# Kernel tuning notes

Hardware: AMD Instinct MI355X
Metric: run time of the kernel (lower is better)

Reference implementation:

```python
import jax, jax.numpy as jnp
import numpy as np

D_MODEL = 1024
NUM_HEADS = 16
D_K = D_MODEL // NUM_HEADS
LN_EPS = 1e-5


def setup_inputs() -> dict:
    key = jax.random.key(0)
    ks = jax.random.split(key, 10)
    s = 1.0 / np.sqrt(D_MODEL)
    x = jax.random.normal(ks[0], (4, 2048, D_MODEL), dtype=jnp.float32)
    Wq = jax.random.uniform(ks[1], (D_MODEL, D_MODEL), jnp.float32, -s, s)
    bq = jax.random.uniform(ks[2], (D_MODEL,), jnp.float32, -s, s)
    Wk = jax.random.uniform(ks[3], (D_MODEL, D_MODEL), jnp.float32, -s, s)
    bk = jax.random.uniform(ks[4], (D_MODEL,), jnp.float32, -s, s)
    Wv = jax.random.uniform(ks[5], (D_MODEL, D_MODEL), jnp.float32, -s, s)
    bv = jax.random.uniform(ks[6], (D_MODEL,), jnp.float32, -s, s)
    Wo = jax.random.uniform(ks[7], (D_MODEL, D_MODEL), jnp.float32, -s, s)
    bo = jax.random.uniform(ks[8], (D_MODEL,), jnp.float32, -s, s)
    gamma = jnp.ones((D_MODEL,), jnp.float32)
    beta = jnp.zeros((D_MODEL,), jnp.float32)
    return {"x": x, "Wq": Wq, "bq": bq, "Wk": Wk, "bk": bk, "Wv": Wv,
            "bv": bv, "Wo": Wo, "bo": bo, "gamma": gamma, "beta": beta}


def reference(x, Wq, bq, Wk, bk, Wv, bv, Wo, bo, gamma, beta):
    B, S, D = x.shape
    H, dk = NUM_HEADS, D_K
    # torch Linear: y = x @ W.T + b
    def proj(W, b):
        y = jnp.einsum('bsd,ed->bse', x, W) + b
        return y.reshape(B, S, H, dk).transpose(0, 2, 1, 3)  # [B,H,S,dk]
    Q = proj(Wq, bq)
    K = proj(Wk, bk)
    V = proj(Wv, bv)
    scores = jnp.einsum('bhqd,bhkd->bhqk', Q, K) / np.sqrt(dk)
    attn = jax.nn.softmax(scores, axis=-1)
    head = jnp.einsum('bhqk,bhkd->bhqd', attn, V)
    head = head.transpose(0, 2, 1, 3).reshape(B, S, D)
    out = jnp.einsum('bsd,ed->bse', head, Wo) + bo
    # LayerNorm
    mu = jnp.mean(out, axis=-1, keepdims=True)
    var = jnp.var(out, axis=-1, keepdims=True)
    out = (out - mu) * jax.lax.rsqrt(var + LN_EPS) * gamma + beta
    # dropout is identity in eval mode
    return x + out
```

## Files before the change

kernel.cpp:

```cpp
#include <hip/hip_runtime.h>
#include <stdint.h>

typedef unsigned short u16;
typedef unsigned int u32;
typedef __attribute__((ext_vector_type(8))) short short8;
typedef __attribute__((ext_vector_type(4))) short short4b;
typedef __attribute__((ext_vector_type(4))) float f32x4;
typedef __attribute__((ext_vector_type(4))) unsigned short u16x4;

#define DEV static __device__ __forceinline__

DEV float bf2f(u16 b) { return __uint_as_float(((uint32_t)b) << 16); }
DEV u16 f2bf(float f) {
  uint32_t u = __float_as_uint(f);
  u += 0x7FFFu + ((u >> 16) & 1u);
  return (u16)(u >> 16);
}
DEV void gld16(const u16* gsrc, u16* ldsdst) {
  __builtin_amdgcn_global_load_lds((const __attribute__((address_space(1))) void*)gsrc,
                                   (__attribute__((address_space(3))) void*)ldsdst, 16, 0, 0);
}
#define MFMA16(a, b, c) __builtin_amdgcn_mfma_f32_16x16x32_bf16(a, b, c, 0, 0, 0)

#define WAITVM4() asm volatile("s_waitcnt vmcnt(4)" ::: "memory")
#define WAITVM0() asm volatile("s_waitcnt vmcnt(0)" ::: "memory")
DEV void barrier() {
  asm volatile("" ::: "memory");
  __builtin_amdgcn_s_barrier();
  asm volatile("" ::: "memory");
}

#if __has_builtin(__builtin_amdgcn_mfma_f32_16x16x16bf16_1k)
DEV f32x4 mfma_k16(short4b a, short4b b, f32x4 c) {
  return __builtin_amdgcn_mfma_f32_16x16x16bf16_1k(a, b, c, 0, 0, 0);
}
#else
DEV f32x4 mfma_k16(short4b a, short4b b, f32x4 c) {
  f32x4 d;
  asm volatile("v_mfma_f32_16x16x16_bf16 %0, %1, %2, %3"
               : "=&v"(d) : "v"(a), "v"(b), "v"(c));
  return d;
}
#endif

#if __has_builtin(__builtin_amdgcn_exp2f)
DEV float fexp2(float x) { return __builtin_amdgcn_exp2f(x); }
#else
DEV float fexp2(float x) { return exp2f(x); }
#endif

DEV u32 cvtpk(float lo, float hi) {
  u32 r;
  asm("v_cvt_pk_bf16_f32 %0, %1, %2" : "=v"(r) : "v"(lo), "v"(hi));
  return r;
}

DEV f32x4 v4max(f32x4 a, f32x4 b) {
  f32x4 r;
  r.x = fmaxf(a.x, b.x); r.y = fmaxf(a.y, b.y);
  r.z = fmaxf(a.z, b.z); r.w = fmaxf(a.w, b.w);
  return r;
}

__global__ __launch_bounds__(256) void k_convert(
    const float* __restrict__ x, const float* __restrict__ wq, const float* __restrict__ wk,
    const float* __restrict__ wv, const float* __restrict__ wo, u16* __restrict__ ws)
{
  int bid = blockIdx.x, t = threadIdx.x;
  const float* src; u16* dst; size_t off;
  if (bid < 8192) { src = x; dst = ws; off = (size_t)bid * 1024; }
  else {
    int r = bid - 8192; int sel = r >> 10; int lb = r & 1023;
    src = sel == 0 ? wq : sel == 1 ? wk : sel == 2 ? wv : wo;
    dst = ws + 8388608u + (size_t)sel * 1048576u;
    off = (size_t)lb * 1024;
  }
  size_t e = off + (size_t)t * 4;
  f32x4 v = *(const f32x4*)(src + e);
  u16x4 o;
  o.x = f2bf(v.x); o.y = f2bf(v.y); o.z = f2bf(v.z); o.w = f2bf(v.w);
  *(u16x4*)(dst + e) = o;
}

DEV void gemm_mainloop(const u16* __restrict__ A, const u16* __restrict__ B,
                       int m0, int n0, u16* As, u16* Bs, f32x4 acc[4][4])
{
  const int tid = threadIdx.x, lane = tid & 63, w = tid >> 6;
  const int fr = lane & 15, g = lane >> 4;
  const int wm = w >> 1, wn = w & 1;

  const int rowA0 = (w * 2 + 0) * 16 + (lane >> 2);
  const int rowA1 = (w * 2 + 1) * 16 + (lane >> 2);
  const int ci = lane & 3;
  const u16* ga0 = A + (size_t)(m0 + rowA0) * 1024 + ((ci ^ (rowA0 & 3)) << 3);
  const u16* ga1 = A + (size_t)(m0 + rowA1) * 1024 + ((ci ^ (rowA1 & 3)) << 3);
  const u16* gb0 = B + (size_t)(n0 + rowA0) * 1024 + ((ci ^ (rowA0 & 3)) << 3);
  const u16* gb1 = B + (size_t)(n0 + rowA1) * 1024 + ((ci ^ (rowA1 & 3)) << 3);
  u16* lA0 = As + (w * 2 + 0) * 512;
  u16* lA1 = As + (w * 2 + 1) * 512;
  u16* lB0 = Bs + (w * 2 + 0) * 512;
  u16* lB1 = Bs + (w * 2 + 1) * 512;

  int raf[4], rbf[4];
#pragma unroll
  for (int i = 0; i < 4; ++i) {
    int rA = wm * 64 + i * 16 + fr;
    raf[i] = rA * 32 + ((g ^ (rA & 3)) << 3);
    int rB = wn * 64 + i * 16 + fr;
    rbf[i] = rB * 32 + ((g ^ (rB & 3)) << 3);
  }

  for (int k0 = 0; k0 < 1024; k0 += 32) {
    __syncthreads();
    gld16(ga0 + k0, lA0);
    gld16(ga1 + k0, lA1);
    gld16(gb0 + k0, lB0);
    gld16(gb1 + k0, lB1);
    __syncthreads();
    short8 af[4], bf[4];
#pragma unroll
    for (int i = 0; i < 4; ++i) af[i] = *(const short8*)&As[raf[i]];
#pragma unroll
    for (int i = 0; i < 4; ++i) bf[i] = *(const short8*)&Bs[rbf[i]];
#pragma unroll
    for (int mi = 0; mi < 4; ++mi)
#pragma unroll
      for (int ni = 0; ni < 4; ++ni)
        acc[mi][ni] = MFMA16(af[mi], bf[ni], acc[mi][ni]);
  }
}

__global__ __launch_bounds__(256) void k_gemm_qkv(
    const u16* __restrict__ xb, const u16* __restrict__ wqb, const u16* __restrict__ wkb,
    const u16* __restrict__ wvb, const float* __restrict__ bq, const float* __restrict__ bk,
    const float* __restrict__ bv, u16* __restrict__ Qg, u16* __restrict__ Kg,
    u16* __restrict__ Vtg)
{
  __shared__ u16 As[128 * 32], Bs[128 * 32];
  const int mb = blockIdx.x, nb_all = blockIdx.y;
  const int mat = nb_all >> 3, nb = nb_all & 7;
  const u16* W = mat == 0 ? wqb : (mat == 1 ? wkb : wvb);
  const float* bias = mat == 0 ? bq : (mat == 1 ? bk : bv);
  const int m0 = mb * 128, n0 = nb * 128;

  f32x4 acc[4][4];
  f32x4 z = {0.f, 0.f, 0.f, 0.f};
#pragma unroll
  for (int i = 0; i < 4; ++i)
#pragma unroll
    for (int j = 0; j < 4; ++j) acc[i][j] = z;

  gemm_mainloop(xb, W, m0, n0, As, Bs, acc);

  const int tid = threadIdx.x, lane = tid & 63, w = tid >> 6;
  const int fr = lane & 15, g = lane >> 4;
  const int wm = w >> 1, wn = w & 1;

  if (mat <= 1) {
    u16* Og = mat == 0 ? Qg : Kg;
    const float scale = mat == 0 ? 0.18033688011112042f : 1.0f;
#pragma unroll
    for (int mi = 0; mi < 4; ++mi)
#pragma unroll
      for (int ni = 0; ni < 4; ++ni) {
        int n = n0 + wn * 64 + ni * 16 + fr;
        float bv_ = bias[n];
        int h = n >> 6, d = n & 63;
#pragma unroll
        for (int r = 0; r < 4; ++r) {
          int m = m0 + wm * 64 + mi * 16 + 4 * g + r;
          int b = m >> 11, s = m & 2047;
          float v = (acc[mi][ni][r] + bv_) * scale;
          Og[(((size_t)(b * 16 + h)) * 2048 + (size_t)s) * 64 + d] = f2bf(v);
        }
      }
  } else {
#pragma unroll
    for (int mi = 0; mi < 4; ++mi)
#pragma unroll
      for (int ni = 0; ni < 4; ++ni) {
        int n = n0 + wn * 64 + ni * 16 + fr;
        float bv_ = bias[n];
        int h = n >> 6, d = n & 63;
        int mbase = m0 + wm * 64 + mi * 16 + 4 * g;
        int b = mbase >> 11, s0 = mbase & 2047;
        u16x4 pk;
        pk.x = f2bf(acc[mi][ni][0] + bv_);
        pk.y = f2bf(acc[mi][ni][1] + bv_);
        pk.z = f2bf(acc[mi][ni][2] + bv_);
        pk.w = f2bf(acc[mi][ni][3] + bv_);
        *(u16x4*)&Vtg[(((size_t)(b * 16 + h)) * 64 + d) * 2048 + s0] = pk;
      }
  }
}

__global__ __launch_bounds__(512, 1) void k_attn(
    const u16* __restrict__ Qg, const u16* __restrict__ Kg, const u16* __restrict__ Vtg,
    u16* __restrict__ headb)
{
  __shared__ u16 K_lds[2][128 * 64];
  __shared__ u16 V_lds[2][64 * 128];
  const int tid = threadIdx.x, lane = tid & 63, w = tid >> 6;
  const int fr = lane & 15, g = lane >> 4;
  const int swz = ((blockIdx.x & 7) << 6) + (blockIdx.x >> 3);
  const int qb = swz & 7, bh = swz >> 3;
  const u16* Qbase = Qg + (size_t)bh * 2048 * 64;
  const u16* Kbase = Kg + (size_t)bh * 2048 * 64;
  const u16* Vbase = Vtg + (size_t)bh * 64 * 2048;

  const int ck0 = w * 2, ck1 = w * 2 + 1;
  const int krow0 = ck0 * 8 + (lane >> 3), krow1 = ck1 * 8 + (lane >> 3);
  const int kci = lane & 7;
  const u16* gk0 = Kbase + (size_t)krow0 * 64 + ((kci ^ (krow0 & 7)) << 3);
  const u16* gk1 = Kbase + (size_t)krow1 * 64 + ((kci ^ (krow1 & 7)) << 3);
  const int vrow0 = ck0 * 4 + (lane >> 4), vrow1 = ck1 * 4 + (lane >> 4);
  const int vci = lane & 15;
  const u16* gv0 = Vbase + (size_t)vrow0 * 2048 + ((vci ^ (vrow0 & 7)) << 3);
  const u16* gv1 = Vbase + (size_t)vrow1 * 2048 + ((vci ^ (vrow1 & 7)) << 3);

  short8 qf[2][2];
#pragma unroll
  for (int mi = 0; mi < 2; ++mi)
#pragma unroll
    for (int kt = 0; kt < 2; ++kt) {
      int qrow = qb * 256 + w * 32 + mi * 16 + fr;
      qf[mi][kt] = *(const short8*)&Qbase[(size_t)qrow * 64 + kt * 32 + g * 8];
    }

  f32x4 po[2][4];
  f32x4 z = {0.f, 0.f, 0.f, 0.f};
#pragma unroll
  for (int mi = 0; mi < 2; ++mi)
#pragma unroll
    for (int dt = 0; dt < 4; ++dt) po[mi][dt] = z;
  float mrun[2] = {-1e30f, -1e30f};
  float lrun[2] = {0.f, 0.f};

  gld16(gk0, K_lds[0] + ck0 * 512);
  gld16(gk1, K_lds[0] + ck1 * 512);
  gld16(gv0, V_lds[0] + ck0 * 512);
  gld16(gv1, V_lds[0] + ck1 * 512);

  for (int kv = 0; kv < 16; ++kv) {
    const int cur = kv & 1;
    if (kv < 15) {
      const int ko = (kv + 1) * 128 * 64;
      const int vo = (kv + 1) * 128;
      gld16(gk0 + ko, K_lds[cur ^ 1] + ck0 * 512);
      gld16(gk1 + ko, K_lds[cur ^ 1] + ck1 * 512);
      gld16(gv0 + vo, V_lds[cur ^ 1] + ck0 * 512);
      gld16(gv1 + vo, V_lds[cur ^ 1] + ck1 * 512);
      WAITVM4();
    } else {
      WAITVM0();
    }
    barrier();
    const u16* Kc = K_lds[cur];
    const u16* Vc = V_lds[cur];

    f32x4 sc[2][8];
#pragma unroll
    for (int mi = 0; mi < 2; ++mi)
#pragma unroll
      for (int nt = 0; nt < 8; ++nt) sc[mi][nt] = z;
    __builtin_amdgcn_s_setprio(1);
#pragma unroll
    for (int nt = 0; nt < 8; ++nt) {
      int rk = nt * 16 + fr;
#pragma unroll
      for (int kt = 0; kt < 2; ++kt) {
        short8 kb = *(const short8*)&Kc[rk * 64 + (((kt * 4 + g) ^ (rk & 7)) << 3)];
        sc[0][nt] = MFMA16(kb, qf[0][kt], sc[0][nt]);
        sc[1][nt] = MFMA16(kb, qf[1][kt], sc[1][nt]);
      }
    }
    __builtin_amdgcn_s_setprio(0);

    short4b pa[2][8];
#pragma unroll
    for (int mi = 0; mi < 2; ++mi) {
      f32x4 m4 = sc[mi][0];
#pragma unroll
      for (int nt = 1; nt < 8; ++nt) m4 = v4max(m4, sc[mi][nt]);
      float mx = fmaxf(fmaxf(m4.x, m4.y), fmaxf(m4.z, m4.w));
      mx = fmaxf(mx, __shfl_xor(mx, 16, 64));
      mx = fmaxf(mx, __shfl_xor(mx, 32, 64));
      const bool defer = __all(mx - mrun[mi] <= 8.0f);
      const float mnew = defer ? mrun[mi] : mx;
      f32x4 s4 = z;
#pragma unroll
      for (int nt = 0; nt < 8; ++nt) {
        f32x4 p;
        p.x = fexp2(sc[mi][nt].x - mnew);
        p.y = fexp2(sc[mi][nt].y - mnew);
        p.z = fexp2(sc[mi][nt].z - mnew);
        p.w = fexp2(sc[mi][nt].w - mnew);
        sc[mi][nt] = p;
        s4 += p;
      }
      float rs = (s4.x + s4.y) + (s4.z + s4.w);
      rs += __shfl_xor(rs, 16, 64);
      rs += __shfl_xor(rs, 32, 64);
      if (defer) {
        lrun[mi] += rs;
      } else {
        float alpha = fexp2(mrun[mi] - mnew);
        lrun[mi] = lrun[mi] * alpha + rs;
        mrun[mi] = mnew;
        f32x4 al4;
#pragma unroll
        for (int r = 0; r < 4; ++r) al4[r] = __shfl(alpha, 4 * g + r, 64);
#pragma unroll
        for (int dt = 0; dt < 4; ++dt) po[mi][dt] *= al4;
      }
#pragma unroll
      for (int nt = 0; nt < 8; ++nt) {
        union { u32 u[2]; short4b s; } cv;
        cv.u[0] = cvtpk(sc[mi][nt].x, sc[mi][nt].y);
        cv.u[1] = cvtpk(sc[mi][nt].z, sc[mi][nt].w);
        pa[mi][nt] = cv.s;
      }
    }

    __builtin_amdgcn_s_setprio(1);
#pragma unroll
    for (int nt = 0; nt < 8; ++nt) {
#pragma unroll
      for (int dt = 0; dt < 4; ++dt) {
        int d = dt * 16 + fr;
        short4b vb = *(const short4b*)&Vc[d * 128 + ((((nt << 1) | (g >> 1)) ^ (d & 7)) << 3) + ((g & 1) << 2)];
        po[0][dt] = mfma_k16(pa[0][nt], vb, po[0][dt]);
        po[1][dt] = mfma_k16(pa[1][nt], vb, po[1][dt]);
      }
    }
    __builtin_amdgcn_s_setprio(0);
    barrier();
  }

  float linv[2][4];
#pragma unroll
  for (int mi = 0; mi < 2; ++mi)
#pragma unroll
    for (int r = 0; r < 4; ++r)
      linv[mi][r] = 1.0f / __shfl(lrun[mi], 4 * g + r, 64);

  const int b = bh >> 4, h = bh & 15;
#pragma unroll
  for (int mi = 0; mi < 2; ++mi)
#pragma unroll
    for (int dt = 0; dt < 4; ++dt)
#pragma unroll
      for (int r = 0; r < 4; ++r) {
        int srow = qb * 256 + w * 32 + mi * 16 + 4 * g + r;
        float v = po[mi][dt][r] * linv[mi][r];
        int e = h * 64 + dt * 16 + fr;
        headb[((size_t)(b * 2048 + srow)) * 1024 + e] = f2bf(v);
      }
}

__global__ __launch_bounds__(256) void k_gemm_o(
    const u16* __restrict__ headb, const u16* __restrict__ wob, const float* __restrict__ bo,
    u16* __restrict__ projb)
{
  __shared__ u16 As[128 * 32], Bs[128 * 32];
  const int m0 = blockIdx.x * 128, n0 = blockIdx.y * 128;
  f32x4 acc[4][4];
  f32x4 z = {0.f, 0.f, 0.f, 0.f};
#pragma unroll
  for (int i = 0; i < 4; ++i)
#pragma unroll
    for (int j = 0; j < 4; ++j) acc[i][j] = z;

  gemm_mainloop(headb, wob, m0, n0, As, Bs, acc);

  const int tid = threadIdx.x, lane = tid & 63, w = tid >> 6;
  const int fr = lane & 15, g = lane >> 4;
  const int wm = w >> 1, wn = w & 1;
#pragma unroll
  for (int mi = 0; mi < 4; ++mi)
#pragma unroll
    for (int ni = 0; ni < 4; ++ni) {
      int n = n0 + wn * 64 + ni * 16 + fr;
      float bv_ = bo[n];
#pragma unroll
      for (int r = 0; r < 4; ++r) {
        int m = m0 + wm * 64 + mi * 16 + 4 * g + r;
        projb[(size_t)m * 1024 + n] = f2bf(acc[mi][ni][r] + bv_);
      }
    }
}

__global__ __launch_bounds__(256) void k_ln(
    const u16* __restrict__ projb, const float* __restrict__ x,
    const float* __restrict__ gamma, const float* __restrict__ beta, float* __restrict__ out)
{
  __shared__ float sh1[4], sh2[4];
  const int row = blockIdx.x, t = threadIdx.x, lane = t & 63, w = t >> 6;
  const size_t base = (size_t)row * 1024;
  u16x4 pv = *(const u16x4*)&projb[base + t * 4];
  float v0 = bf2f(pv.x), v1 = bf2f(pv.y), v2 = bf2f(pv.z), v3 = bf2f(pv.w);
  float s1 = v0 + v1 + v2 + v3;
  float s2 = v0 * v0 + v1 * v1 + v2 * v2 + v3 * v3;
  for (int m = 1; m < 64; m <<= 1) {
    s1 += __shfl_xor(s1, m, 64);
    s2 += __shfl_xor(s2, m, 64);
  }
  if (lane == 0) { sh1[w] = s1; sh2[w] = s2; }
  __syncthreads();
  s1 = sh1[0] + sh1[1] + sh1[2] + sh1[3];
  s2 = sh2[0] + sh2[1] + sh2[2] + sh2[3];
  float mu = s1 * (1.0f / 1024.0f);
  float var = s2 * (1.0f / 1024.0f) - mu * mu;
  float rsd = rsqrtf(var + 1e-5f);
  f32x4 xv = *(const f32x4*)&x[base + t * 4];
  f32x4 res;
  int e = t * 4;
  res.x = xv.x + (v0 - mu) * rsd * gamma[e + 0] + beta[e + 0];
  res.y = xv.y + (v1 - mu) * rsd * gamma[e + 1] + beta[e + 1];
  res.z = xv.z + (v2 - mu) * rsd * gamma[e + 2] + beta[e + 2];
  res.w = xv.w + (v3 - mu) * rsd * gamma[e + 3] + beta[e + 3];
  *(f32x4*)&out[base + t * 4] = res;
}

extern "C" void kernel_launch(void* const* d_in, const int* in_sizes, int n_in,
                              void* d_out, int out_size, void* d_ws, size_t ws_size,
                              hipStream_t stream)
{
  const float* x     = (const float*)d_in[0];
  const float* Wq    = (const float*)d_in[1];
  const float* bq    = (const float*)d_in[2];
  const float* Wk    = (const float*)d_in[3];
  const float* bk    = (const float*)d_in[4];
  const float* Wv    = (const float*)d_in[5];
  const float* bv    = (const float*)d_in[6];
  const float* Wo    = (const float*)d_in[7];
  const float* bo    = (const float*)d_in[8];
  const float* gamma = (const float*)d_in[9];
  const float* beta  = (const float*)d_in[10];
  float* out = (float*)d_out;

  u16* ws   = (u16*)d_ws;
  u16* xb   = ws;
  u16* wqb  = ws + 8388608;
  u16* wkb  = wqb + 1048576;
  u16* wvb  = wkb + 1048576;
  u16* wob  = wvb + 1048576;
  u16* Qg   = wob + 1048576;
  u16* Kg   = Qg + 8388608;
  u16* Vtg  = Kg + 8388608;
  u16* headb = Vtg + 8388608;
  u16* projb = Qg;

  k_convert<<<12288, 256, 0, stream>>>(x, Wq, Wk, Wv, Wo, ws);
  k_gemm_qkv<<<dim3(64, 24), 256, 0, stream>>>(xb, wqb, wkb, wvb, bq, bk, bv, Qg, Kg, Vtg);
  k_attn<<<dim3(512), 512, 0, stream>>>(Qg, Kg, Vtg, headb);
  k_gemm_o<<<dim3(64, 8), 256, 0, stream>>>(headb, wob, bo, projb);
  k_ln<<<8192, 256, 0, stream>>>(projb, x, gamma, beta, out);
}
```

Measured before the change: 241.7 us.

## Rewrite attention kernel with 32x32x16 MFMA and smaller 64-key tiles

Moves the flash-attention kernel from 16x16 MFMA tiles to 32x32x16 bf16 MFMA. Each wave now owns 32 query rows, so row max and sum reductions need only one cross-half shuffle, and the P fragments are rebuilt through a lane-xor exchange. Blocks shrink to 256 threads with 128 queries each, the KV tile drops to 64 keys, and the grid doubles to 1024 blocks. The aim is fewer MFMA issues and less softmax shuffle overhead, plus higher occupancy. The cost is twice as many KV-loop iterations and barriers, and extra shuffles to repack P.

```diff
diff --git a/kernel.cpp b/kernel.cpp
--- a/kernel.cpp
+++ b/kernel.cpp
@@ -4,8 +4,8 @@
 typedef unsigned short u16;
 typedef unsigned int u32;
 typedef __attribute__((ext_vector_type(8))) short short8;
-typedef __attribute__((ext_vector_type(4))) short short4b;
 typedef __attribute__((ext_vector_type(4))) float f32x4;
+typedef __attribute__((ext_vector_type(16))) float f32x16;
 typedef __attribute__((ext_vector_type(4))) unsigned short u16x4;
 
 #define DEV static __device__ __forceinline__
@@ -21,6 +21,7 @@
                                    (__attribute__((address_space(3))) void*)ldsdst, 16, 0, 0);
 }
 #define MFMA16(a, b, c) __builtin_amdgcn_mfma_f32_16x16x32_bf16(a, b, c, 0, 0, 0)
+#define MFMA32(a, b, c) __builtin_amdgcn_mfma_f32_32x32x16_bf16(a, b, c, 0, 0, 0)
 
 #define WAITVM4() asm volatile("s_waitcnt vmcnt(4)" ::: "memory")
 #define WAITVM0() asm volatile("s_waitcnt vmcnt(0)" ::: "memory")
@@ -30,19 +31,6 @@
   asm volatile("" ::: "memory");
 }
 
-#if __has_builtin(__builtin_amdgcn_mfma_f32_16x16x16bf16_1k)
-DEV f32x4 mfma_k16(short4b a, short4b b, f32x4 c) {
-  return __builtin_amdgcn_mfma_f32_16x16x16bf16_1k(a, b, c, 0, 0, 0);
-}
-#else
-DEV f32x4 mfma_k16(short4b a, short4b b, f32x4 c) {
-  f32x4 d;
-  asm volatile("v_mfma_f32_16x16x16_bf16 %0, %1, %2, %3"
-               : "=&v"(d) : "v"(a), "v"(b), "v"(c));
-  return d;
-}
-#endif
-
 #if __has_builtin(__builtin_amdgcn_exp2f)
 DEV float fexp2(float x) { return __builtin_amdgcn_exp2f(x); }
 #else
@@ -52,13 +40,6 @@
 DEV u32 cvtpk(float lo, float hi) {
   u32 r;
   asm("v_cvt_pk_bf16_f32 %0, %1, %2" : "=v"(r) : "v"(lo), "v"(hi));
-  return r;
-}
-
-DEV f32x4 v4max(f32x4 a, f32x4 b) {
-  f32x4 r;
-  r.x = fmaxf(a.x, b.x); r.y = fmaxf(a.y, b.y);
-  r.z = fmaxf(a.z, b.z); r.w = fmaxf(a.w, b.w);
   return r;
 }
 
@@ -194,58 +175,57 @@
   }
 }
 
-__global__ __launch_bounds__(512, 1) void k_attn(
+__global__ __launch_bounds__(256) void k_attn(
     const u16* __restrict__ Qg, const u16* __restrict__ Kg, const u16* __restrict__ Vtg,
     u16* __restrict__ headb)
 {
-  __shared__ u16 K_lds[2][128 * 64];
-  __shared__ u16 V_lds[2][64 * 128];
+  __shared__ u16 K_lds[2][64 * 64];
+  __shared__ u16 V_lds[2][64 * 64];
   const int tid = threadIdx.x, lane = tid & 63, w = tid >> 6;
-  const int fr = lane & 15, g = lane >> 4;
-  const int swz = ((blockIdx.x & 7) << 6) + (blockIdx.x >> 3);
-  const int qb = swz & 7, bh = swz >> 3;
+  const int l31 = lane & 31, h5 = lane >> 5, k7 = lane & 7;
+  const bool lo_half = (h5 == 0);
+  const int swz = ((blockIdx.x & 7) << 7) + (blockIdx.x >> 3);
+  const int qb = swz & 15, bh = swz >> 4;
   const u16* Qbase = Qg + (size_t)bh * 2048 * 64;
   const u16* Kbase = Kg + (size_t)bh * 2048 * 64;
   const u16* Vbase = Vtg + (size_t)bh * 64 * 2048;
 
   const int ck0 = w * 2, ck1 = w * 2 + 1;
-  const int krow0 = ck0 * 8 + (lane >> 3), krow1 = ck1 * 8 + (lane >> 3);
-  const int kci = lane & 7;
-  const u16* gk0 = Kbase + (size_t)krow0 * 64 + ((kci ^ (krow0 & 7)) << 3);
-  const u16* gk1 = Kbase + (size_t)krow1 * 64 + ((kci ^ (krow1 & 7)) << 3);
-  const int vrow0 = ck0 * 4 + (lane >> 4), vrow1 = ck1 * 4 + (lane >> 4);
-  const int vci = lane & 15;
-  const u16* gv0 = Vbase + (size_t)vrow0 * 2048 + ((vci ^ (vrow0 & 7)) << 3);
-  const u16* gv1 = Vbase + (size_t)vrow1 * 2048 + ((vci ^ (vrow1 & 7)) << 3);
-
-  short8 qf[2][2];
-#pragma unroll
-  for (int mi = 0; mi < 2; ++mi)
-#pragma unroll
-    for (int kt = 0; kt < 2; ++kt) {
-      int qrow = qb * 256 + w * 32 + mi * 16 + fr;
-      qf[mi][kt] = *(const short8*)&Qbase[(size_t)qrow * 64 + kt * 32 + g * 8];
-    }
-
-  f32x4 po[2][4];
-  f32x4 z = {0.f, 0.f, 0.f, 0.f};
-#pragma unroll
-  for (int mi = 0; mi < 2; ++mi)
-#pragma unroll
-    for (int dt = 0; dt < 4; ++dt) po[mi][dt] = z;
-  float mrun[2] = {-1e30f, -1e30f};
-  float lrun[2] = {0.f, 0.f};
+  const int srow0 = ck0 * 8 + (lane >> 3), srow1 = ck1 * 8 + (lane >> 3);
+  const int sci = lane & 7;
+  const u16* gk0 = Kbase + (size_t)srow0 * 64 + ((sci ^ (srow0 & 7)) << 3);
+  const u16* gk1 = Kbase + (size_t)srow1 * 64 + ((sci ^ (srow1 & 7)) << 3);
+  const u16* gv0 = Vbase + (size_t)srow0 * 2048 + ((sci ^ (srow0 & 7)) << 3);
+  const u16* gv1 = Vbase + (size_t)srow1 * 2048 + ((sci ^ (srow1 & 7)) << 3);
+
+  short8 qf[4];
+  {
+    const u16* qrow = Qbase + (size_t)(qb * 128 + w * 32 + l31) * 64;
+#pragma unroll
+    for (int j = 0; j < 4; ++j)
+      qf[j] = *(const short8*)&qrow[j * 16 + h5 * 8];
+  }
+
+  int cj[4];
+#pragma unroll
+  for (int j = 0; j < 4; ++j) cj[j] = (((2 * j + h5) ^ k7) << 3);
+  const int rb = l31 * 64;
+
+  f32x16 po0, po1;
+#pragma unroll
+  for (int e = 0; e < 16; ++e) { po0[e] = 0.f; po1[e] = 0.f; }
+  float mrun = -1e30f, lrun = 0.f;
 
   gld16(gk0, K_lds[0] + ck0 * 512);
   gld16(gk1, K_lds[0] + ck1 * 512);
   gld16(gv0, V_lds[0] + ck0 * 512);
   gld16(gv1, V_lds[0] + ck1 * 512);
 
-  for (int kv = 0; kv < 16; ++kv) {
+  for (int kv = 0; kv < 32; ++kv) {
     const int cur = kv & 1;
-    if (kv < 15) {
-      const int ko = (kv + 1) * 128 * 64;
-      const int vo = (kv + 1) * 128;
+    if (kv < 31) {
+      const int ko = (kv + 1) * 64 * 64;
+      const int vo = (kv + 1) * 64;
       gld16(gk0 + ko, K_lds[cur ^ 1] + ck0 * 512);
       gld16(gk1 + ko, K_lds[cur ^ 1] + ck1 * 512);
       gld16(gv0 + vo, V_lds[cur ^ 1] + ck0 * 512);
@@ -258,104 +238,99 @@
     const u16* Kc = K_lds[cur];
     const u16* Vc = V_lds[cur];
 
-    f32x4 sc[2][8];
-#pragma unroll
-    for (int mi = 0; mi < 2; ++mi)
-#pragma unroll
-      for (int nt = 0; nt < 8; ++nt) sc[mi][nt] = z;
+    f32x16 s0, s1;
+#pragma unroll
+    for (int e = 0; e < 16; ++e) { s0[e] = 0.f; s1[e] = 0.f; }
     __builtin_amdgcn_s_setprio(1);
 #pragma unroll
-    for (int nt = 0; nt < 8; ++nt) {
-      int rk = nt * 16 + fr;
-#pragma unroll
-      for (int kt = 0; kt < 2; ++kt) {
-        short8 kb = *(const short8*)&Kc[rk * 64 + (((kt * 4 + g) ^ (rk & 7)) << 3)];
-        sc[0][nt] = MFMA16(kb, qf[0][kt], sc[0][nt]);
-        sc[1][nt] = MFMA16(kb, qf[1][kt], sc[1][nt]);
-      }
+    for (int j = 0; j < 4; ++j) {
+      short8 kf0 = *(const short8*)&Kc[rb + cj[j]];
+      short8 kf1 = *(const short8*)&Kc[2048 + rb + cj[j]];
+      s0 = MFMA32(kf0, qf[j], s0);
+      s1 = MFMA32(kf1, qf[j], s1);
     }
     __builtin_amdgcn_s_setprio(0);
 
-    short4b pa[2][8];
-#pragma unroll
-    for (int mi = 0; mi < 2; ++mi) {
-      f32x4 m4 = sc[mi][0];
-#pragma unroll
-      for (int nt = 1; nt < 8; ++nt) m4 = v4max(m4, sc[mi][nt]);
-      float mx = fmaxf(fmaxf(m4.x, m4.y), fmaxf(m4.z, m4.w));
-      mx = fmaxf(mx, __shfl_xor(mx, 16, 64));
-      mx = fmaxf(mx, __shfl_xor(mx, 32, 64));
-      const bool defer = __all(mx - mrun[mi] <= 8.0f);
-      const float mnew = defer ? mrun[mi] : mx;
-      f32x4 s4 = z;
-#pragma unroll
-      for (int nt = 0; nt < 8; ++nt) {
-        f32x4 p;
-        p.x = fexp2(sc[mi][nt].x - mnew);
-        p.y = fexp2(sc[mi][nt].y - mnew);
-        p.z = fexp2(sc[mi][nt].z - mnew);
-        p.w = fexp2(sc[mi][nt].w - mnew);
-        sc[mi][nt] = p;
-        s4 += p;
-      }
-      float rs = (s4.x + s4.y) + (s4.z + s4.w);
-      rs += __shfl_xor(rs, 16, 64);
-      rs += __shfl_xor(rs, 32, 64);
-      if (defer) {
-        lrun[mi] += rs;
-      } else {
-        float alpha = fexp2(mrun[mi] - mnew);
-        lrun[mi] = lrun[mi] * alpha + rs;
-        mrun[mi] = mnew;
-        f32x4 al4;
-#pragma unroll
-        for (int r = 0; r < 4; ++r) al4[r] = __shfl(alpha, 4 * g + r, 64);
-#pragma unroll
-        for (int dt = 0; dt < 4; ++dt) po[mi][dt] *= al4;
-      }
-#pragma unroll
-      for (int nt = 0; nt < 8; ++nt) {
-        union { u32 u[2]; short4b s; } cv;
-        cv.u[0] = cvtpk(sc[mi][nt].x, sc[mi][nt].y);
-        cv.u[1] = cvtpk(sc[mi][nt].z, sc[mi][nt].w);
-        pa[mi][nt] = cv.s;
-      }
+    float mx = fmaxf(s0[0], s1[0]);
+#pragma unroll
+    for (int e = 1; e < 16; ++e) mx = fmaxf(mx, fmaxf(s0[e], s1[e]));
+    mx = fmaxf(mx, __shfl_xor(mx, 32, 64));
+    const bool defer = __all(mx - mrun <= 8.0f);
+    const float mnew = defer ? mrun : mx;
+#pragma unroll
+    for (int e = 0; e < 16; ++e) {
+      s0[e] = fexp2(s0[e] - mnew);
+      s1[e] = fexp2(s1[e] - mnew);
+    }
+    float a0 = 0.f, a1 = 0.f, a2 = 0.f, a3 = 0.f;
+#pragma unroll
+    for (int e = 0; e < 4; ++e) {
+      a0 += s0[4 * e + 0] + s1[4 * e + 0];
+      a1 += s0[4 * e + 1] + s1[4 * e + 1];
+      a2 += s0[4 * e + 2] + s1[4 * e + 2];
+      a3 += s0[4 * e + 3] + s1[4 * e + 3];
+    }
+    float rs = (a0 + a1) + (a2 + a3);
+    rs += __shfl_xor(rs, 32, 64);
+    if (defer) {
+      lrun += rs;
+    } else {
+      float alpha = fexp2(mrun - mnew);
+      lrun = lrun * alpha + rs;
+      mrun = mnew;
+#pragma unroll
+      for (int e = 0; e < 16; ++e) { po0[e] *= alpha; po1[e] *= alpha; }
     }
 
     __builtin_amdgcn_s_setprio(1);
 #pragma unroll
-    for (int nt = 0; nt < 8; ++nt) {
-#pragma unroll
-      for (int dt = 0; dt < 4; ++dt) {
-        int d = dt * 16 + fr;
-        short4b vb = *(const short4b*)&Vc[d * 128 + ((((nt << 1) | (g >> 1)) ^ (d & 7)) << 3) + ((g & 1) << 2)];
-        po[0][dt] = mfma_k16(pa[0][nt], vb, po[0][dt]);
-        po[1][dt] = mfma_k16(pa[1][nt], vb, po[1][dt]);
-      }
+    for (int s = 0; s < 4; ++s) {
+      u32 lo0, lo1, hi0, hi1;
+      if (s == 0)      { lo0 = cvtpk(s0[0], s0[1]);  lo1 = cvtpk(s0[2], s0[3]);
+                         hi0 = cvtpk(s0[4], s0[5]);  hi1 = cvtpk(s0[6], s0[7]); }
+      else if (s == 1) { lo0 = cvtpk(s0[8], s0[9]);  lo1 = cvtpk(s0[10], s0[11]);
+                         hi0 = cvtpk(s0[12], s0[13]); hi1 = cvtpk(s0[14], s0[15]); }
+      else if (s == 2) { lo0 = cvtpk(s1[0], s1[1]);  lo1 = cvtpk(s1[2], s1[3]);
+                         hi0 = cvtpk(s1[4], s1[5]);  hi1 = cvtpk(s1[6], s1[7]); }
+      else             { lo0 = cvtpk(s1[8], s1[9]);  lo1 = cvtpk(s1[10], s1[11]);
+                         hi0 = cvtpk(s1[12], s1[13]); hi1 = cvtpk(s1[14], s1[15]); }
+      u32 sent0 = lo_half ? hi0 : lo0;
+      u32 sent1 = lo_half ? hi1 : lo1;
+      u32 r0 = __shfl_xor(sent0, 32, 64);
+      u32 r1 = __shfl_xor(sent1, 32, 64);
+      union { u32 u[4]; short8 v; } pf;
+      pf.u[0] = lo_half ? lo0 : r0;
+      pf.u[1] = lo_half ? lo1 : r1;
+      pf.u[2] = lo_half ? r0 : hi0;
+      pf.u[3] = lo_half ? r1 : hi1;
+      short8 vf0 = *(const short8*)&Vc[rb + cj[s]];
+      short8 vf1 = *(const short8*)&Vc[2048 + rb + cj[s]];
+      po0 = MFMA32(vf0, pf.v, po0);
+      po1 = MFMA32(vf1, pf.v, po1);
     }
     __builtin_amdgcn_s_setprio(0);
     barrier();
   }
 
-  float linv[2][4];
-#pragma unroll
-  for (int mi = 0; mi < 2; ++mi)
-#pragma unroll
-    for (int r = 0; r < 4; ++r)
-      linv[mi][r] = 1.0f / __shfl(lrun[mi], 4 * g + r, 64);
-
+  const float linv = 1.0f / lrun;
   const int b = bh >> 4, h = bh & 15;
-#pragma unroll
-  for (int mi = 0; mi < 2; ++mi)
-#pragma unroll
-    for (int dt = 0; dt < 4; ++dt)
-#pragma unroll
-      for (int r = 0; r < 4; ++r) {
-        int srow = qb * 256 + w * 32 + mi * 16 + 4 * g + r;
-        float v = po[mi][dt][r] * linv[mi][r];
-        int e = h * 64 + dt * 16 + fr;
-        headb[((size_t)(b * 2048 + srow)) * 1024 + e] = f2bf(v);
-      }
+  const int srow = qb * 128 + w * 32 + l31;
+  u16* rowp = headb + (size_t)(b * 2048 + srow) * 1024 + h * 64;
+#pragma unroll
+  for (int i = 0; i < 4; ++i) {
+    u16x4 pk;
+    pk.x = f2bf(po0[4 * i + 0] * linv);
+    pk.y = f2bf(po0[4 * i + 1] * linv);
+    pk.z = f2bf(po0[4 * i + 2] * linv);
+    pk.w = f2bf(po0[4 * i + 3] * linv);
+    *(u16x4*)&rowp[8 * i + 4 * h5] = pk;
+    u16x4 pk2;
+    pk2.x = f2bf(po1[4 * i + 0] * linv);
+    pk2.y = f2bf(po1[4 * i + 1] * linv);
+    pk2.z = f2bf(po1[4 * i + 2] * linv);
+    pk2.w = f2bf(po1[4 * i + 3] * linv);
+    *(u16x4*)&rowp[32 + 8 * i + 4 * h5] = pk2;
+  }
 }
 
 __global__ __launch_bounds__(256) void k_gemm_o(
@@ -453,7 +428,7 @@
 
   k_convert<<<12288, 256, 0, stream>>>(x, Wq, Wk, Wv, Wo, ws);
   k_gemm_qkv<<<dim3(64, 24), 256, 0, stream>>>(xb, wqb, wkb, wvb, bq, bk, bv, Qg, Kg, Vtg);
-  k_attn<<<dim3(512), 512, 0, stream>>>(Qg, Kg, Vtg, headb);
+  k_attn<<<dim3(1024), 256, 0, stream>>>(Qg, Kg, Vtg, headb);
   k_gemm_o<<<dim3(64, 8), 256, 0, stream>>>(headb, wob, bo, projb);
   k_ln<<<8192, 256, 0, stream>>>(projb, x, gamma, beta, out);
 }
```

Result: no change. 241.8 us (+0.1%).
